# Performance work log

Hardware: AMD Instinct MI355X
Metric: run time of the kernel (lower is better)

Reference implementation:

```python
import jax, jax.numpy as jnp
import numpy as np
import math

B_GRAPHS = 256
L_NODES = 64
N_NODES = B_GRAPHS * L_NODES
N_EDGES = N_NODES * 4
HEADS = 8
D_INNER = 512
N_DAGS = 1
DIAMETER = 64


def setup_inputs() -> dict:
    key = jax.random.key(0)
    ks = jax.random.split(key, 8)
    x = jax.random.normal(ks[0], (N_NODES, D_INNER), jnp.float32)
    B = jax.random.normal(ks[1], (N_NODES, D_INNER), jnp.float32)
    C = jax.random.normal(ks[2], (N_NODES, D_INNER), jnp.float32)
    dt = jax.random.normal(ks[3], (N_NODES, N_DAGS * HEADS * 2), jnp.float32)
    dt_edge = jax.random.normal(ks[4], (N_EDGES, N_DAGS * HEADS), jnp.float32)
    # DAG edges: within each graph, src_local < dst_local (gap 1..7) -> strictly upper triangular
    u = jax.random.randint(ks[5], (N_EDGES,), 0, L_NODES - 1)
    gap = jax.random.randint(ks[6], (N_EDGES,), 1, 8)
    v = jnp.minimum(u + gap, L_NODES - 1)
    graph = jnp.arange(N_EDGES) // (N_EDGES // B_GRAPHS)
    edge_index = jnp.stack([graph * L_NODES + u, graph * L_NODES + v]).astype(jnp.int32)
    data_batch = (jnp.arange(N_NODES) // L_NODES).astype(jnp.int32)
    dag_masks = jnp.ones((N_DAGS, N_EDGES), jnp.float32)
    # dt_bias init as in module __init__ (inverse softplus of dt in [1e-3, 1e-1])
    rng = np.random.default_rng(0)
    dtv = np.exp(rng.uniform(size=(HEADS,)) * (math.log(0.1) - math.log(0.001)) + math.log(0.001))
    dtv = np.clip(dtv, 1e-4, None)
    dt_bias = jnp.asarray(dtv + np.log(-np.expm1(-dtv)), jnp.float32)
    D = jnp.ones((HEADS,), jnp.float32)
    return dict(x=x, B=B, C=C, dt=dt, dt_edge=dt_edge, dt_bias=dt_bias, D=D,
                dag_masks=dag_masks, edge_index=edge_index, data_batch=data_batch,
                diameter=DIAMETER)


def _repeated_squaring_inverse(A, diam):
    # (I - A)^{-1} = prod_k (I + A^{2^k}) for nilpotent A; O(log diam) matmuls
    j = 2 ** int(math.ceil(math.log2(diam)))
    I = jnp.eye(A.shape[-1], dtype=A.dtype)
    last = A
    M = I + A
    for _ in range(2, int(math.log2(j)) + 1):
        last = last @ last
        M = M @ (I + last)
    return M


def reference(x, B, C, dt, dt_edge, dt_bias, D, dag_masks, edge_index, data_batch, diameter):
    N, din = x.shape
    g, E = dag_masks.shape
    n = dt_bias.shape[0]
    b = int(data_batch[-1]) + 1
    l = N // b  # equal-size graphs -> dense batching is a reshape, mask all-True
    h = din // n
    src, dst = edge_index[0], edge_index[1]

    # dt_node: (N, g*n*c) -> (c, g, n, N); softplus(dt + bias)
    c = dt.shape[1] // (g * n)
    dtn = dt.reshape(N, g, n, c).transpose(3, 1, 2, 0)
    dtn = jax.nn.softplus(dtn + dt_bias[None, None, :, None])
    dte = dt_edge.reshape(E, g, n).transpose(1, 2, 0)  # (g,n,E)
    dte = jax.nn.softplus(dte + dt_bias[None, :, None])

    dt_s, dt_t = dtn[0], dtn[1]
    dt_sum = (dt_s[:, :, src] + dt_t[:, :, dst] + dte) / np.sqrt(3.0)  # (g,n,E)
    dt_exp = jnp.exp(-dt_sum)
    msk = dag_masks[:, None, :]
    dt_sum = dt_sum * msk
    dt_exp = dt_exp * msk

    # dense adjacency with per-edge attrs; note 'b l1 l2 (g n) -> b g n l2 l1' transpose
    b_e = src // l
    sl = src % l
    dl = dst % l
    attr = dt_exp.transpose(2, 0, 1).reshape(E, g * n)
    adj = jnp.zeros((b, l, l, g * n), x.dtype).at[b_e, sl, dl].add(attr)
    A = adj.reshape(b, l, l, g, n).transpose(0, 3, 4, 2, 1)  # (b,g,n,l,l)

    # normalize_mat: sqrt outer product of in-degree counts, clamped at 1
    ec = jnp.zeros((g, N), x.dtype).at[:, dst].add(dag_masks)
    ec_dense = ec.T.reshape(b, l, g)
    outer = jnp.sqrt(jnp.einsum('blg,btg->bglt', ec_dense, ec_dense))
    outer = jnp.where(outer < 1.0, 1.0, outer)
    A = A / outer[:, :, None]

    dnorm = jnp.zeros((g, n, N), x.dtype).at[:, :, dst].add(dt_sum)
    dnorm = dnorm.transpose(2, 0, 1).reshape(b, l, g, n).transpose(0, 2, 3, 1)  # (b,g,n,l)

    A2 = A.reshape(b, g * n, l, l).astype(jnp.float32)
    L = _repeated_squaring_inverse(A2, int(diameter))
    L = L.reshape(b, g, n, l, l) * dnorm[..., None]

    x4 = x.reshape(b, l, n, h).transpose(0, 2, 1, 3)  # (b,n,l,h)
    B3 = B.reshape(b, l, -1)
    C3 = C.reshape(b, l, -1)
    # y = einsum(C,L,B,x) with B/C broadcast over (g,n): fold C.B^T into L
    CB = jnp.einsum('bld,btd->blt', C3, B3)
    M = L * CB[:, None, None]
    y = jnp.einsum('bgnlt,bnth->bgnlh', M, x4)
    y = y + x4[:, None] * D[None, None, :, None, None]
    y = y.transpose(0, 3, 1, 2, 4).reshape(N, g, n * h)  # b g n l h -> (N, g, n*h)
    y = y.sum(axis=1) / np.sqrt(g)
    return y
```

## Files before the change

kernel.cpp:

```cpp
#include <hip/hip_runtime.h>
#include <math.h>

#define NGRAPH 256
#define HEADS  8
#define DIN    512
#define EPG    256
#define NEDGE  65536
#define LOG2E 1.44269504088896341f
#define LN2   0.69314718055994531f

typedef short bf16x8 __attribute__((ext_vector_type(8)));
typedef float f32x4 __attribute__((ext_vector_type(4)));

__device__ __forceinline__ float softplusf(float v) {
    if (v > 20.f) return v;
    float t = exp2f(v * LOG2E);
    return LN2 * log2f(1.f + t);
}
__device__ __forceinline__ unsigned short f2bf(float f) {
    union { float f; unsigned u; } c; c.f = f;
    unsigned r = c.u + 0x7fffu + ((c.u >> 16) & 1u);
    return (unsigned short)(r >> 16);
}
__device__ __forceinline__ float bf2f(unsigned short h) {
    union { float f; unsigned u; } c; c.u = ((unsigned)h) << 16;
    return c.f;
}
__device__ __forceinline__ int swz_idx(int row, int t) {
    int g = ((t >> 3) ^ (row ^ (row >> 3))) & 7;
    return (row << 6) | (g << 3) | (t & 7);
}
__device__ __forceinline__ void loadsplit(const float* p, bf16x8& hi, bf16x8& lo) {
    float4 u = *(const float4*)p;
    float4 v = *(const float4*)(p + 4);
    float vv[8] = {u.x, u.y, u.z, u.w, v.x, v.y, v.z, v.w};
    #pragma unroll
    for (int j = 0; j < 8; ++j) {
        union { float f; unsigned q; } c; c.f = vv[j];
        unsigned hb = c.q & 0xffff0000u;
        hi[j] = (short)(unsigned short)(hb >> 16);
        union { float f; unsigned q; } d; d.q = hb;
        union { float f; unsigned q; } e2; e2.f = vv[j] - d.f;
        lo[j] = (short)(unsigned short)(e2.q >> 16);
    }
}

__global__ __launch_bounds__(1024, 4) void dag_ws_v5(
        const float* __restrict__ x,
        const float* __restrict__ Bm,
        const float* __restrict__ Cm,
        const float* __restrict__ dt,
        const float* __restrict__ dt_edge,
        const float* __restrict__ dt_bias,
        const float* __restrict__ Dp,
        const float* __restrict__ dag_masks,
        const int* __restrict__ edge_index,
        float* __restrict__ out) {
    __shared__ __align__(16) unsigned short CBsh[4096];
    __shared__ __align__(16) unsigned short Xt[8][4096];
    __shared__ __align__(16) unsigned short Wl[8][4096];
    __shared__ __align__(16) float Ab8[8][512];
    __shared__ float dts[8][64];
    __shared__ float dtt[8][64];
    __shared__ float ecsh[8][64];

    const int b = blockIdx.x;
    const int tid = threadIdx.x;
    const int w = tid >> 6;
    const int lane = tid & 63;
    const int lm = lane & 15;
    const int quad = lane >> 4;

    if (w < 8) {
        const float bias = dt_bias[w];
        {
            float2 dv = *(const float2*)(dt + ((size_t)(b * 64 + lane)) * 16 + w * 2);
            dts[w][lane] = softplusf(dv.x + bias);
            dtt[w][lane] = softplusf(dv.y + bias);
            ecsh[w][lane] = 0.f;
            float4 z = make_float4(0.f, 0.f, 0.f, 0.f);
            *(float4*)(&Ab8[w][lane * 8]) = z;
            *(float4*)(&Ab8[w][lane * 8 + 4]) = z;
        }
        {
            #pragma unroll
            for (int eo = 0; eo < 4; ++eo) {
                int e = b * EPG + eo * 64 + lane;
                int sl = edge_index[e] & 63;
                int dl = edge_index[NEDGE + e] & 63;
                float mk = dag_masks[e];
                float de = softplusf(dt_edge[(size_t)e * HEADS + w] + bias);
                float dsum = (dts[w][sl] + dtt[w][dl] + de) * 0.57735026918962576451f;
                float dexp = exp2f(-dsum * LOG2E);
                atomicAdd(&Ab8[w][dl * 8 + (dl - sl)], dexp * mk);
                atomicAdd(&Ab8[w][dl * 8], dsum * mk);
                atomicAdd(&ecsh[w][dl], mk);
            }
        }
        {
            const float* xg = x + (size_t)b * 64 * DIN + w * 64;
            #pragma unroll
            for (int r = 0; r < 4; ++r) {
                int t0 = quad * 4 + r * 16;
                int e0 = lm * 4;
                float4 v0 = *(const float4*)(xg + (size_t)(t0 + 0) * DIN + e0);
                float4 v1 = *(const float4*)(xg + (size_t)(t0 + 1) * DIN + e0);
                float4 v2 = *(const float4*)(xg + (size_t)(t0 + 2) * DIN + e0);
                float4 v3 = *(const float4*)(xg + (size_t)(t0 + 3) * DIN + e0);
                float a0[4] = {v0.x, v0.y, v0.z, v0.w};
                float a1[4] = {v1.x, v1.y, v1.z, v1.w};
                float a2[4] = {v2.x, v2.y, v2.z, v2.w};
                float a3[4] = {v3.x, v3.y, v3.z, v3.w};
                #pragma unroll
                for (int k = 0; k < 4; ++k) {
                    unsigned long long pk =
                          (unsigned long long)f2bf(a0[k])
                        | ((unsigned long long)f2bf(a1[k]) << 16)
                        | ((unsigned long long)f2bf(a2[k]) << 32)
                        | ((unsigned long long)f2bf(a3[k]) << 48);
                    *(unsigned long long*)(&Xt[w][swz_idx(e0 + k, t0)]) = pk;
                }
            }
        }
        {
            float eci = ecsh[w][lane];
            float4 a03 = *(const float4*)(&Ab8[w][lane * 8]);
            float4 a47 = *(const float4*)(&Ab8[w][lane * 8 + 4]);
            float sc[7];
            #pragma unroll
            for (int s = 0; s < 7; ++s) {
                int src = lane - 1 - s;
                float p = (src >= 0) ? eci * ecsh[w][src] : 1.f;
                sc[s] = fminf(1.f, rsqrtf(p));
            }
            a03.y *= sc[0]; a03.z *= sc[1]; a03.w *= sc[2];
            a47.x *= sc[3]; a47.y *= sc[4]; a47.z *= sc[5]; a47.w *= sc[6];
            *(float4*)(&Ab8[w][lane * 8]) = a03;
            *(float4*)(&Ab8[w][lane * 8 + 4]) = a47;
        }
    } else {
        const int hw = w - 8;
        const int mi = hw >> 1;
        const int ni0 = (hw & 1) * 2;
        const float* Cr = Cm + ((size_t)(b * 64 + mi * 16 + lm)) * DIN + quad * 8;
        const float* B0 = Bm + ((size_t)(b * 64 + ni0 * 16 + lm)) * DIN + quad * 8;
        const float* B1 = B0 + (size_t)16 * DIN;
        f32x4 acc0 = {0.f, 0.f, 0.f, 0.f};
        f32x4 acc1 = {0.f, 0.f, 0.f, 0.f};
        #pragma unroll 4
        for (int ks = 0; ks < 16; ++ks) {
            bf16x8 ah, al, b0h, b0l, b1h, b1l;
            loadsplit(Cr + ks * 32, ah, al);
            loadsplit(B0 + ks * 32, b0h, b0l);
            loadsplit(B1 + ks * 32, b1h, b1l);
            acc0 = __builtin_amdgcn_mfma_f32_16x16x32_bf16(ah, b0h, acc0, 0, 0, 0);
            acc0 = __builtin_amdgcn_mfma_f32_16x16x32_bf16(ah, b0l, acc0, 0, 0, 0);
            acc0 = __builtin_amdgcn_mfma_f32_16x16x32_bf16(al, b0h, acc0, 0, 0, 0);
            acc1 = __builtin_amdgcn_mfma_f32_16x16x32_bf16(ah, b1h, acc1, 0, 0, 0);
            acc1 = __builtin_amdgcn_mfma_f32_16x16x32_bf16(ah, b1l, acc1, 0, 0, 0);
            acc1 = __builtin_amdgcn_mfma_f32_16x16x32_bf16(al, b1h, acc1, 0, 0, 0);
        }
        #pragma unroll
        for (int r = 0; r < 4; ++r) {
            int row = mi * 16 + quad * 4 + r;
            CBsh[row * 64 + ni0 * 16 + lm] = f2bf(acc0[r]);
            CBsh[row * 64 + (ni0 + 1) * 16 + lm] = f2bf(acc1[r]);
        }
    }

    __syncthreads();

    if (w < 8) {
        const int j = lane;
        const float Dh = Dp[w];
        float mwin[7] = {0.f, 0.f, 0.f, 0.f, 0.f, 0.f, 0.f};
        float4 a03 = *(const float4*)(&Ab8[w][0]);
        float4 a47 = *(const float4*)(&Ab8[w][4]);
        float cbv = bf2f(CBsh[j]);
        #pragma unroll 2
        for (int i = 0; i < 64; ++i) {
            float4 n03, n47;
            float ncb = 0.f;
            if (i < 63) {
                n03 = *(const float4*)(&Ab8[w][(i + 1) * 8]);
                n47 = *(const float4*)(&Ab8[w][(i + 1) * 8 + 4]);
                ncb = bf2f(CBsh[(i + 1) * 64 + j]);
            } else {
                n03 = make_float4(0.f, 0.f, 0.f, 0.f);
                n47 = n03;
            }
            float diag = (j == i) ? 1.f : 0.f;
            float t0 = fmaf(a03.y, mwin[0], fmaf(a03.z, mwin[1], diag));
            float t1 = fmaf(a03.w, mwin[2], fmaf(a47.x, mwin[3], a47.y * mwin[4]));
            float t2 = fmaf(a47.z, mwin[5], a47.w * mwin[6]);
            float mi_ = t0 + (t1 + t2);
            float wv = mi_ * cbv * a03.x;
            if (j == i) wv += Dh;
            Wl[w][swz_idx(i, j)] = f2bf(wv);
            #pragma unroll
            for (int s = 6; s > 0; --s) mwin[s] = mwin[s - 1];
            mwin[0] = mi_;
            a03 = n03; a47 = n47; cbv = ncb;
        }
    }

    __syncthreads();

    {
        const int head = (w < 8) ? w : (w - 8);
        const int m2base = (w < 8) ? 0 : 2;
        bf16x8 bfr[4][2];
        #pragma unroll
        for (int eb = 0; eb < 4; ++eb) {
            int er = eb * 16 + lm;
            bfr[eb][0] = *(const bf16x8*)(&Xt[head][swz_idx(er, quad * 8)]);
            bfr[eb][1] = *(const bf16x8*)(&Xt[head][swz_idx(er, 32 + quad * 8)]);
        }
        float* og = out + ((size_t)b * 64) * DIN + head * 64;
        #pragma unroll
        for (int m2o = 0; m2o < 2; ++m2o) {
            int row0 = (m2base + m2o) * 16 + lm;
            bf16x8 a0 = *(const bf16x8*)(&Wl[head][swz_idx(row0, quad * 8)]);
            bf16x8 a1 = *(const bf16x8*)(&Wl[head][swz_idx(row0, 32 + quad * 8)]);
            f32x4 acc[4];
            #pragma unroll
            for (int eb = 0; eb < 4; ++eb) {
                f32x4 z = {0.f, 0.f, 0.f, 0.f};
                z = __builtin_amdgcn_mfma_f32_16x16x32_bf16(a0, bfr[eb][0], z, 0, 0, 0);
                z = __builtin_amdgcn_mfma_f32_16x16x32_bf16(a1, bfr[eb][1], z, 0, 0, 0);
                acc[eb] = z;
            }
            #pragma unroll
            for (int r = 0; r < 4; ++r) {
                int row = (m2base + m2o) * 16 + quad * 4 + r;
                #pragma unroll
                for (int eb = 0; eb < 4; ++eb)
                    og[(size_t)row * DIN + eb * 16 + lm] = acc[eb][r];
            }
        }
    }
}

extern "C" void kernel_launch(void* const* d_in, const int* in_sizes, int n_in,
                              void* d_out, int out_size, void* d_ws, size_t ws_size,
                              hipStream_t stream) {
    (void)in_sizes; (void)n_in; (void)out_size; (void)d_ws; (void)ws_size;
    dag_ws_v5<<<dim3(NGRAPH), dim3(1024), 0, stream>>>(
        (const float*)d_in[0],
        (const float*)d_in[1],
        (const float*)d_in[2],
        (const float*)d_in[3],
        (const float*)d_in[4],
        (const float*)d_in[5],
        (const float*)d_in[6],
        (const float*)d_in[7],
        (const int*)d_in[8],
        (float*)d_out);
}
```

Before: 176.2 us.

## Merge warp-specialized roles into 512-thread block with double-buffered LDS staging for CB

Drops the split between 8 scan waves and 8 C·B^T waves. All 8 waves now do the edge scatter, x transpose, C·B^T and recurrence, in a 512-thread block. B and C are prefetched into registers, split into bf16 hi/lo and staged through a double-buffered LDS area. Each wave's MFMAs then read from LDS, and x and edge loads are issued early to overlap with this work. The LDS staging buffer is then reused for the per-head W matrices, so the final matmul is done per wave with no block barrier. The cost is more __syncthreads in the CB loop and fewer threads per block.

```diff
diff --git a/kernel.cpp b/kernel.cpp
--- a/kernel.cpp
+++ b/kernel.cpp
@@ -11,6 +11,7 @@
 
 typedef short bf16x8 __attribute__((ext_vector_type(8)));
 typedef float f32x4 __attribute__((ext_vector_type(4)));
+typedef unsigned long long u64;
 
 __device__ __forceinline__ float softplusf(float v) {
     if (v > 20.f) return v;
@@ -30,22 +31,16 @@
     int g = ((t >> 3) ^ (row ^ (row >> 3))) & 7;
     return (row << 6) | (g << 3) | (t & 7);
 }
-__device__ __forceinline__ void loadsplit(const float* p, bf16x8& hi, bf16x8& lo) {
-    float4 u = *(const float4*)p;
-    float4 v = *(const float4*)(p + 4);
-    float vv[8] = {u.x, u.y, u.z, u.w, v.x, v.y, v.z, v.w};
-    #pragma unroll
-    for (int j = 0; j < 8; ++j) {
-        union { float f; unsigned q; } c; c.f = vv[j];
-        unsigned hb = c.q & 0xffff0000u;
-        hi[j] = (short)(unsigned short)(hb >> 16);
-        union { float f; unsigned q; } d; d.q = hb;
-        union { float f; unsigned q; } e2; e2.f = vv[j] - d.f;
-        lo[j] = (short)(unsigned short)(e2.q >> 16);
-    }
-}
-
-__global__ __launch_bounds__(1024, 4) void dag_ws_v5(
+__device__ __forceinline__ void split1(float f, unsigned short& hi, unsigned short& lo) {
+    union { float f; unsigned q; } c; c.f = f;
+    unsigned hb = c.q & 0xffff0000u;
+    hi = (unsigned short)(hb >> 16);
+    union { float f; unsigned q; } d; d.q = hb;
+    union { float f; unsigned q; } e2; e2.f = f - d.f;
+    lo = (unsigned short)(e2.q >> 16);
+}
+
+__global__ __launch_bounds__(512, 2) void dag_pipe_v6(
         const float* __restrict__ x,
         const float* __restrict__ Bm,
         const float* __restrict__ Cm,
@@ -56,13 +51,13 @@
         const float* __restrict__ dag_masks,
         const int* __restrict__ edge_index,
         float* __restrict__ out) {
+    __shared__ __align__(16) unsigned short WS[32768];
+    __shared__ __align__(16) unsigned short Xt[HEADS][4096];
     __shared__ __align__(16) unsigned short CBsh[4096];
-    __shared__ __align__(16) unsigned short Xt[8][4096];
-    __shared__ __align__(16) unsigned short Wl[8][4096];
-    __shared__ __align__(16) float Ab8[8][512];
-    __shared__ float dts[8][64];
-    __shared__ float dtt[8][64];
-    __shared__ float ecsh[8][64];
+    __shared__ __align__(16) float Ab8[HEADS][512];
+    __shared__ float dts[HEADS][64];
+    __shared__ float dtt[HEADS][64];
+    __shared__ float ecsh[HEADS][64];
 
     const int b = blockIdx.x;
     const int tid = threadIdx.x;
@@ -70,89 +65,105 @@
     const int lane = tid & 63;
     const int lm = lane & 15;
     const int quad = lane >> 4;
-
-    if (w < 8) {
-        const float bias = dt_bias[w];
-        {
-            float2 dv = *(const float2*)(dt + ((size_t)(b * 64 + lane)) * 16 + w * 2);
-            dts[w][lane] = softplusf(dv.x + bias);
-            dtt[w][lane] = softplusf(dv.y + bias);
-            ecsh[w][lane] = 0.f;
-            float4 z = make_float4(0.f, 0.f, 0.f, 0.f);
-            *(float4*)(&Ab8[w][lane * 8]) = z;
-            *(float4*)(&Ab8[w][lane * 8 + 4]) = z;
-        }
-        {
-            #pragma unroll
-            for (int eo = 0; eo < 4; ++eo) {
-                int e = b * EPG + eo * 64 + lane;
-                int sl = edge_index[e] & 63;
-                int dl = edge_index[NEDGE + e] & 63;
-                float mk = dag_masks[e];
-                float de = softplusf(dt_edge[(size_t)e * HEADS + w] + bias);
-                float dsum = (dts[w][sl] + dtt[w][dl] + de) * 0.57735026918962576451f;
-                float dexp = exp2f(-dsum * LOG2E);
-                atomicAdd(&Ab8[w][dl * 8 + (dl - sl)], dexp * mk);
-                atomicAdd(&Ab8[w][dl * 8], dsum * mk);
-                atomicAdd(&ecsh[w][dl], mk);
-            }
-        }
-        {
-            const float* xg = x + (size_t)b * 64 * DIN + w * 64;
-            #pragma unroll
-            for (int r = 0; r < 4; ++r) {
-                int t0 = quad * 4 + r * 16;
-                int e0 = lm * 4;
-                float4 v0 = *(const float4*)(xg + (size_t)(t0 + 0) * DIN + e0);
-                float4 v1 = *(const float4*)(xg + (size_t)(t0 + 1) * DIN + e0);
-                float4 v2 = *(const float4*)(xg + (size_t)(t0 + 2) * DIN + e0);
-                float4 v3 = *(const float4*)(xg + (size_t)(t0 + 3) * DIN + e0);
-                float a0[4] = {v0.x, v0.y, v0.z, v0.w};
-                float a1[4] = {v1.x, v1.y, v1.z, v1.w};
-                float a2[4] = {v2.x, v2.y, v2.z, v2.w};
-                float a3[4] = {v3.x, v3.y, v3.z, v3.w};
-                #pragma unroll
-                for (int k = 0; k < 4; ++k) {
-                    unsigned long long pk =
-                          (unsigned long long)f2bf(a0[k])
-                        | ((unsigned long long)f2bf(a1[k]) << 16)
-                        | ((unsigned long long)f2bf(a2[k]) << 32)
-                        | ((unsigned long long)f2bf(a3[k]) << 48);
-                    *(unsigned long long*)(&Xt[w][swz_idx(e0 + k, t0)]) = pk;
-                }
-            }
-        }
-        {
-            float eci = ecsh[w][lane];
-            float4 a03 = *(const float4*)(&Ab8[w][lane * 8]);
-            float4 a47 = *(const float4*)(&Ab8[w][lane * 8 + 4]);
-            float sc[7];
-            #pragma unroll
-            for (int s = 0; s < 7; ++s) {
-                int src = lane - 1 - s;
-                float p = (src >= 0) ? eci * ecsh[w][src] : 1.f;
-                sc[s] = fminf(1.f, rsqrtf(p));
-            }
-            a03.y *= sc[0]; a03.z *= sc[1]; a03.w *= sc[2];
-            a47.x *= sc[3]; a47.y *= sc[4]; a47.z *= sc[5]; a47.w *= sc[6];
-            *(float4*)(&Ab8[w][lane * 8]) = a03;
-            *(float4*)(&Ab8[w][lane * 8 + 4]) = a47;
-        }
-    } else {
-        const int hw = w - 8;
-        const int mi = hw >> 1;
-        const int ni0 = (hw & 1) * 2;
-        const float* Cr = Cm + ((size_t)(b * 64 + mi * 16 + lm)) * DIN + quad * 8;
-        const float* B0 = Bm + ((size_t)(b * 64 + ni0 * 16 + lm)) * DIN + quad * 8;
-        const float* B1 = B0 + (size_t)16 * DIN;
-        f32x4 acc0 = {0.f, 0.f, 0.f, 0.f};
-        f32x4 acc1 = {0.f, 0.f, 0.f, 0.f};
-        #pragma unroll 4
-        for (int ks = 0; ks < 16; ++ks) {
-            bf16x8 ah, al, b0h, b0l, b1h, b1l;
-            loadsplit(Cr + ks * 32, ah, al);
-            loadsplit(B0 + ks * 32, b0h, b0l);
-            loadsplit(B1 + ks * 32, b1h, b1l);
+    const float bias = dt_bias[w];
+
+    float2 dv = *(const float2*)(dt + ((size_t)(b * 64 + lane)) * 16 + w * 2);
+
+    const int u0 = tid * 4;
+    const int mat = u0 >> 10;
+    const int srow = (u0 & 1023) >> 4;
+    const int scol = (u0 & 15) << 2;
+    const float* sp = (mat ? Bm : Cm) + ((size_t)(b * 64 + srow)) * DIN + scol;
+
+    float4 pre0[4], pre1[4];
+    #pragma unroll
+    for (int i = 0; i < 4; ++i) pre0[i] = *(const float4*)(sp + 0 * 64 + 4 * i);
+    #pragma unroll
+    for (int i = 0; i < 4; ++i) pre1[i] = *(const float4*)(sp + 1 * 64 + 4 * i);
+
+    int esl[4], edl[4]; float emk[4], edr[4];
+    #pragma unroll
+    for (int eo = 0; eo < 4; ++eo) {
+        int e = b * EPG + eo * 64 + lane;
+        esl[eo] = edge_index[e];
+        edl[eo] = edge_index[NEDGE + e];
+        emk[eo] = dag_masks[e];
+        edr[eo] = dt_edge[(size_t)e * HEADS + w];
+    }
+
+    float4 xv[16];
+    const float* xg = x + (size_t)b * 64 * DIN + w * 64;
+    #pragma unroll
+    for (int r = 0; r < 4; ++r) {
+        int t0 = quad * 4 + r * 16;
+        #pragma unroll
+        for (int k = 0; k < 4; ++k)
+            xv[r * 4 + k] = *(const float4*)(xg + (size_t)(t0 + k) * DIN + lm * 4);
+    }
+
+    dts[w][lane] = softplusf(dv.x + bias);
+    dtt[w][lane] = softplusf(dv.y + bias);
+    ecsh[w][lane] = 0.f;
+    {
+        float4 z = make_float4(0.f, 0.f, 0.f, 0.f);
+        *(float4*)(&Ab8[w][lane * 8]) = z;
+        *(float4*)(&Ab8[w][lane * 8 + 4]) = z;
+    }
+
+    #pragma unroll
+    for (int eo = 0; eo < 4; ++eo) {
+        int sl = esl[eo] & 63;
+        int dl = edl[eo] & 63;
+        float de = softplusf(edr[eo] + bias);
+        float dsum = (dts[w][sl] + dtt[w][dl] + de) * 0.57735026918962576451f;
+        float dexp = exp2f(-dsum * LOG2E);
+        atomicAdd(&Ab8[w][dl * 8 + (dl - sl)], dexp * emk[eo]);
+        atomicAdd(&Ab8[w][dl * 8], dsum * emk[eo]);
+        atomicAdd(&ecsh[w][dl], emk[eo]);
+    }
+
+    const int mi = w >> 1;
+    const int ni0 = (w & 1) * 2;
+    f32x4 acc0 = {0.f, 0.f, 0.f, 0.f};
+    f32x4 acc1 = {0.f, 0.f, 0.f, 0.f};
+    #pragma unroll
+    for (int c = 0; c < 8; ++c) {
+        unsigned short* buf = WS + (c & 1) * 16384;
+        unsigned short* thi = buf + mat * 8192;
+        #pragma unroll
+        for (int i = 0; i < 4; ++i) {
+            float4 v = (c & 1) ? pre1[i] : pre0[i];
+            float a[4] = {v.x, v.y, v.z, v.w};
+            u64 hp = 0, lp = 0;
+            #pragma unroll
+            for (int k = 0; k < 4; ++k) {
+                unsigned short h, l;
+                split1(a[k], h, l);
+                hp |= ((u64)h) << (16 * k);
+                lp |= ((u64)l) << (16 * k);
+            }
+            int idx = swz_idx(srow, scol + 4 * i);
+            *(u64*)(thi + idx) = hp;
+            *(u64*)(thi + 4096 + idx) = lp;
+        }
+        if (c + 2 < 8) {
+            #pragma unroll
+            for (int i = 0; i < 4; ++i) {
+                float4 nv = *(const float4*)(sp + (c + 2) * 64 + 4 * i);
+                if (c & 1) pre1[i] = nv; else pre0[i] = nv;
+            }
+        }
+        __syncthreads();
+        const unsigned short* p = buf;
+        #pragma unroll
+        for (int ks = 0; ks < 2; ++ks) {
+            int kl = ks * 32 + quad * 8;
+            bf16x8 ah  = *(const bf16x8*)(p +         swz_idx(mi * 16 + lm, kl));
+            bf16x8 al  = *(const bf16x8*)(p +  4096 + swz_idx(mi * 16 + lm, kl));
+            bf16x8 b0h = *(const bf16x8*)(p +  8192 + swz_idx(ni0 * 16 + lm, kl));
+            bf16x8 b0l = *(const bf16x8*)(p + 12288 + swz_idx(ni0 * 16 + lm, kl));
+            bf16x8 b1h = *(const bf16x8*)(p +  8192 + swz_idx((ni0 + 1) * 16 + lm, kl));
+            bf16x8 b1l = *(const bf16x8*)(p + 12288 + swz_idx((ni0 + 1) * 16 + lm, kl));
             acc0 = __builtin_amdgcn_mfma_f32_16x16x32_bf16(ah, b0h, acc0, 0, 0, 0);
             acc0 = __builtin_amdgcn_mfma_f32_16x16x32_bf16(ah, b0l, acc0, 0, 0, 0);
             acc0 = __builtin_amdgcn_mfma_f32_16x16x32_bf16(al, b0h, acc0, 0, 0, 0);
@@ -160,17 +171,55 @@
             acc1 = __builtin_amdgcn_mfma_f32_16x16x32_bf16(ah, b1l, acc1, 0, 0, 0);
             acc1 = __builtin_amdgcn_mfma_f32_16x16x32_bf16(al, b1h, acc1, 0, 0, 0);
         }
+    }
+    #pragma unroll
+    for (int r = 0; r < 4; ++r) {
+        int row = mi * 16 + quad * 4 + r;
+        CBsh[row * 64 + ni0 * 16 + lm] = f2bf(acc0[r]);
+        CBsh[row * 64 + (ni0 + 1) * 16 + lm] = f2bf(acc1[r]);
+    }
+
+    {
+        int e0 = lm * 4;
         #pragma unroll
         for (int r = 0; r < 4; ++r) {
-            int row = mi * 16 + quad * 4 + r;
-            CBsh[row * 64 + ni0 * 16 + lm] = f2bf(acc0[r]);
-            CBsh[row * 64 + (ni0 + 1) * 16 + lm] = f2bf(acc1[r]);
+            int t0 = quad * 4 + r * 16;
+            float A0[4] = {xv[r*4+0].x, xv[r*4+0].y, xv[r*4+0].z, xv[r*4+0].w};
+            float A1[4] = {xv[r*4+1].x, xv[r*4+1].y, xv[r*4+1].z, xv[r*4+1].w};
+            float A2[4] = {xv[r*4+2].x, xv[r*4+2].y, xv[r*4+2].z, xv[r*4+2].w};
+            float A3[4] = {xv[r*4+3].x, xv[r*4+3].y, xv[r*4+3].z, xv[r*4+3].w};
+            #pragma unroll
+            for (int k = 0; k < 4; ++k) {
+                u64 pk = (u64)f2bf(A0[k])
+                       | ((u64)f2bf(A1[k]) << 16)
+                       | ((u64)f2bf(A2[k]) << 32)
+                       | ((u64)f2bf(A3[k]) << 48);
+                *(u64*)(&Xt[w][swz_idx(e0 + k, t0)]) = pk;
+            }
         }
     }
 
     __syncthreads();
 
-    if (w < 8) {
+    {
+        float eci = ecsh[w][lane];
+        float4 a03 = *(const float4*)(&Ab8[w][lane * 8]);
+        float4 a47 = *(const float4*)(&Ab8[w][lane * 8 + 4]);
+        float sc[7];
+        #pragma unroll
+        for (int s = 0; s < 7; ++s) {
+            int src = lane - 1 - s;
+            float p = (src >= 0) ? eci * ecsh[w][src] : 1.f;
+            sc[s] = fminf(1.f, rsqrtf(p));
+        }
+        a03.y *= sc[0]; a03.z *= sc[1]; a03.w *= sc[2];
+        a47.x *= sc[3]; a47.y *= sc[4]; a47.z *= sc[5]; a47.w *= sc[6];
+        *(float4*)(&Ab8[w][lane * 8]) = a03;
+        *(float4*)(&Ab8[w][lane * 8 + 4]) = a47;
+    }
+
+    unsigned short* Wlw = WS + w * 4096;
+    {
         const int j = lane;
         const float Dh = Dp[w];
         float mwin[7] = {0.f, 0.f, 0.f, 0.f, 0.f, 0.f, 0.f};
@@ -196,7 +245,7 @@
             float mi_ = t0 + (t1 + t2);
             float wv = mi_ * cbv * a03.x;
             if (j == i) wv += Dh;
-            Wl[w][swz_idx(i, j)] = f2bf(wv);
+            Wlw[swz_idx(i, j)] = f2bf(wv);
             #pragma unroll
             for (int s = 6; s > 0; --s) mwin[s] = mwin[s - 1];
             mwin[0] = mi_;
@@ -204,24 +253,20 @@
         }
     }
 
-    __syncthreads();
-
-    {
-        const int head = (w < 8) ? w : (w - 8);
-        const int m2base = (w < 8) ? 0 : 2;
+    {
         bf16x8 bfr[4][2];
         #pragma unroll
         for (int eb = 0; eb < 4; ++eb) {
             int er = eb * 16 + lm;
-            bfr[eb][0] = *(const bf16x8*)(&Xt[head][swz_idx(er, quad * 8)]);
-            bfr[eb][1] = *(const bf16x8*)(&Xt[head][swz_idx(er, 32 + quad * 8)]);
-        }
-        float* og = out + ((size_t)b * 64) * DIN + head * 64;
-        #pragma unroll
-        for (int m2o = 0; m2o < 2; ++m2o) {
-            int row0 = (m2base + m2o) * 16 + lm;
-            bf16x8 a0 = *(const bf16x8*)(&Wl[head][swz_idx(row0, quad * 8)]);
-            bf16x8 a1 = *(const bf16x8*)(&Wl[head][swz_idx(row0, 32 + quad * 8)]);
+            bfr[eb][0] = *(const bf16x8*)(&Xt[w][swz_idx(er, quad * 8)]);
+            bfr[eb][1] = *(const bf16x8*)(&Xt[w][swz_idx(er, 32 + quad * 8)]);
+        }
+        float* og = out + ((size_t)b * 64) * DIN + w * 64;
+        #pragma unroll
+        for (int m2 = 0; m2 < 4; ++m2) {
+            int row0 = m2 * 16 + lm;
+            bf16x8 a0 = *(const bf16x8*)(&Wlw[swz_idx(row0, quad * 8)]);
+            bf16x8 a1 = *(const bf16x8*)(&Wlw[swz_idx(row0, 32 + quad * 8)]);
             f32x4 acc[4];
             #pragma unroll
             for (int eb = 0; eb < 4; ++eb) {
@@ -232,7 +277,7 @@
             }
             #pragma unroll
             for (int r = 0; r < 4; ++r) {
-                int row = (m2base + m2o) * 16 + quad * 4 + r;
+                int row = m2 * 16 + quad * 4 + r;
                 #pragma unroll
                 for (int eb = 0; eb < 4; ++eb)
                     og[(size_t)row * DIN + eb * 16 + lm] = acc[eb][r];
@@ -245,7 +290,7 @@
                               void* d_out, int out_size, void* d_ws, size_t ws_size,
                               hipStream_t stream) {
     (void)in_sizes; (void)n_in; (void)out_size; (void)d_ws; (void)ws_size;
-    dag_ws_v5<<<dim3(NGRAPH), dim3(1024), 0, stream>>>(
+    dag_pipe_v6<<<dim3(NGRAPH), dim3(512), 0, stream>>>(
         (const float*)d_in[0],
         (const float*)d_in[1],
         (const float*)d_in[2],
```

New measurement: 163.6 us. -7.2%, faster.
